# Kernel tuning notes

Measured on AMD Instinct MI355X. Metric: run time of the kernel, lower is better.

## Reference

```python
import jax, jax.numpy as jnp
import numpy as np

B, T, D = 2, 2048, 2048
H, KVH = 16, 4
HD = D // H            # 128 head_dim
D1 = HD // 2           # 64 tied (no-rope) dims
D2 = HD - D1           # 64 rope dims
REP = H // KVH         # 4 kv repeats
ROPE_BASE = 10000.0
EPS = 1e-6
LAMBDA_INIT = 0.8 - 0.6 * float(np.exp(-0.3 * 0))  # layer_depth=0 -> 0.2


def setup_inputs() -> dict:
    key = jax.random.key(0)
    ks = jax.random.split(key, 8)
    x = jax.random.normal(ks[0], (B, T, D), jnp.float32)
    W_qkv = jax.random.normal(ks[1], (D, (H + KVH) * HD), jnp.float32) * 0.02
    W_rope_k = jax.random.normal(ks[2], (D, D2), jnp.float32) * 0.02
    b_rope_k = jnp.zeros((D2,), jnp.float32)
    softmax_scaler = jnp.ones((H,), jnp.float32)
    lambda_q1 = jax.random.normal(ks[3], (D1,), jnp.float32) * 0.1
    lambda_k1 = jax.random.normal(ks[4], (D1,), jnp.float32) * 0.1
    lambda_q2 = jax.random.normal(ks[5], (D1,), jnp.float32) * 0.1
    lambda_k2 = jax.random.normal(ks[6], (D1,), jnp.float32) * 0.1
    return {"hidden_states": x, "W_qkv": W_qkv, "W_rope_k": W_rope_k,
            "b_rope_k": b_rope_k, "softmax_scaler": softmax_scaler,
            "lambda_q1": lambda_q1, "lambda_k1": lambda_k1,
            "lambda_q2": lambda_q2, "lambda_k2": lambda_k2}


def _rmsnorm(x):
    return x * jax.lax.rsqrt(jnp.mean(x * x, axis=-1, keepdims=True) + EPS)


def _rope_tables(seq_len):
    inv_freq = 1.0 / ROPE_BASE ** (jnp.arange(0, D2, 2, dtype=jnp.float32) / D2)
    t = jnp.arange(seq_len, dtype=jnp.float32)
    freqs = jnp.outer(t, inv_freq)          # [T, D2/2]
    return jnp.cos(freqs), jnp.sin(freqs)


def _apply_rotary(x, cos, sin):
    # x: [B, T, h, D2]; cos/sin: [T, D2/2]
    d = x.shape[-1] // 2
    x1, x2 = x[..., :d], x[..., d:]
    c = cos[None, :, None, :]
    s = sin[None, :, None, :]
    return jnp.concatenate([x1 * c + x2 * s, -x1 * s + x2 * c], axis=-1)


def _causal_attn(q, k, v):
    # q,k: [B, T, h, HD]; v: [B, T, h, 2*HD]
    scale = 1.0 / jnp.sqrt(jnp.float32(HD))
    scores = jnp.einsum('bthd,bshd->bhts', q, k) * scale
    mask = jnp.arange(T)[:, None] >= jnp.arange(T)[None, :]
    scores = jnp.where(mask[None, None], scores, jnp.float32(-1e30))
    p = jax.nn.softmax(scores, axis=-1)
    return jnp.einsum('bhts,bshd->bthd', p, v)


def reference(hidden_states, W_qkv, W_rope_k, b_rope_k, softmax_scaler,
              lambda_q1, lambda_k1, lambda_q2, lambda_k2):
    x = hidden_states
    qkv = (x @ W_qkv).reshape(B, T, H + KVH, HD)
    qkv = _rmsnorm(qkv)                              # qk_norm (no affine)
    q, kv = qkv[:, :, :H], qkv[:, :, H:]             # [B,T,H,HD], [B,T,KVH,HD]

    q_tied, q_rope = q[..., :D1], q[..., D1:]
    k_rope = (x @ W_rope_k + b_rope_k)[:, :, None, :]          # [B,T,1,D2]
    k_rope = jnp.broadcast_to(k_rope, (B, T, H, D2))

    cos, sin = _rope_tables(T)
    q_rope = _apply_rotary(q_rope, cos, sin)
    k_rope = _apply_rotary(k_rope, cos, sin)
    q = jnp.concatenate([q_tied, q_rope], axis=-1)             # [B,T,H,HD]

    kv_tied, v_hidden = kv[..., :D1], kv[..., D1:]
    kv_tied = jnp.repeat(kv_tied, REP, axis=2)                 # grouped KV
    v_hidden = jnp.repeat(v_hidden, REP, axis=2)
    k = jnp.concatenate([kv_tied, k_rope], axis=-1)            # [B,T,H,HD]
    v = jnp.concatenate([kv_tied, v_hidden], axis=-1)          # [B,T,H,HD]

    # scalable softmax: q <- s_h * log(pos) * q  (full context, wsize=-1)
    pos = jnp.arange(1, T + 1, dtype=jnp.float32)
    q = softmax_scaler[None, None, :, None] * jnp.log(pos)[None, :, None, None] * q

    # differential head pairing
    q1, q2 = q[:, :, 0::2], q[:, :, 1::2]
    k1, k2 = k[:, :, 0::2], k[:, :, 1::2]
    v_pair = v.reshape(B, T, H // 2, 2 * HD)

    y1 = _causal_attn(q1, k1, v_pair)
    y2 = _causal_attn(q2, k2, v_pair)

    lam1 = jnp.exp(jnp.sum(lambda_q1 * lambda_k1))
    lam2 = jnp.exp(jnp.sum(lambda_q2 * lambda_k2))
    lambda_full = lam1 - lam2 + jnp.float32(LAMBDA_INIT)
    y = y1 - lambda_full * y2                                  # [B,T,H/2,2*HD]
    return y
```

## Files before the change

kernel.cpp:

```cpp
#include <hip/hip_runtime.h>

#define TT 2048
#define NQKV 2560

typedef _Float16 f16;
typedef _Float16 f16x8 __attribute__((ext_vector_type(8)));
typedef _Float16 f16x4v __attribute__((ext_vector_type(4)));
typedef _Float16 f16x2 __attribute__((ext_vector_type(2)));
typedef float f32x4 __attribute__((ext_vector_type(4)));

#define GLOBAL_AS(p) ((const __attribute__((address_space(1))) void*)(p))
#define LDS_AS(p)    ((__attribute__((address_space(3))) void*)(p))

__device__ __forceinline__ f32x4 mfma_f16(f16x8 a, f16x8 b, f32x4 c) {
  return __builtin_amdgcn_mfma_f32_16x16x32_f16(a, b, c, 0, 0, 0);
}

__global__ __launch_bounds__(256) void k_cast_f16(const float* __restrict__ in,
                                                  f16* __restrict__ out, int n4) {
  int i = blockIdx.x * 256 + threadIdx.x;
  if (i >= n4) return;
  float4 v = reinterpret_cast<const float4*>(in)[i];
  f16x4v o;
  o[0] = (f16)v.x; o[1] = (f16)v.y; o[2] = (f16)v.z; o[3] = (f16)v.w;
  reinterpret_cast<f16x4v*>(out)[i] = o;
}

__global__ __launch_bounds__(256) void k_transpose_f16(const float* __restrict__ W,
                                                       f16* __restrict__ Wt,
                                                       int K, int N) {
  __shared__ f16 tile[32][33];
  int tx = threadIdx.x & 31, ty = threadIdx.x >> 5;
  int n0 = blockIdx.x * 32, k0 = blockIdx.y * 32;
  #pragma unroll
  for (int i = ty; i < 32; i += 8)
    tile[i][tx] = (f16)W[(size_t)(k0 + i) * N + n0 + tx];
  __syncthreads();
  #pragma unroll
  for (int i = ty; i < 32; i += 8)
    Wt[(size_t)(n0 + i) * K + k0 + tx] = tile[tx][i];
}

template<int BM, int BN, int WGM, int WGN>
__global__ __launch_bounds__(256) void gemm_bt_kernel(
    const f16* __restrict__ A, const f16* __restrict__ Bt,
    f16* __restrict__ C, int M, int N, int K)
{
  constexpr int BK = 32;
  constexpr int WM = BM / WGM, WN = BN / WGN;
  constexpr int FM = WM / 16, FN = WN / 16;
  constexpr int ACH = BM * 4;
  constexpr int TCH = (BM + BN) * 4;
  __shared__ alignas(16) f16 lds[(BM + BN) * BK];
  const int tid = threadIdx.x;
  const int lane = tid & 63;
  const int w = tid >> 6;
  const int l15 = lane & 15, grp = lane >> 4;
  const int wm = w / WGN, wn = w % WGN;
  const int m0 = blockIdx.y * BM, n0 = blockIdx.x * BN;

  f32x4 acc[FM][FN];
  #pragma unroll
  for (int i = 0; i < FM; ++i)
    #pragma unroll
    for (int j = 0; j < FN; ++j)
      acc[i][j] = (f32x4){0.f, 0.f, 0.f, 0.f};

  const int nk = K / BK;
  for (int kt = 0; kt < nk; ++kt) {
    __syncthreads();
    for (int c = tid; c < TCH; c += 256) {
      const f16* gp;
      if (c < ACH) {
        int row = c >> 2;
        gp = A + (size_t)(m0 + row) * K + kt * BK + (c & 3) * 8;
      } else {
        int cc = c - ACH;
        int row = cc >> 2;
        gp = Bt + (size_t)(n0 + row) * K + kt * BK + (cc & 3) * 8;
      }
      __builtin_amdgcn_global_load_lds(GLOBAL_AS(gp),
                                       LDS_AS((char*)lds + (size_t)c * 16),
                                       16, 0, 0);
    }
    __syncthreads();
    f16x8 af[FM], bfr[FN];
    #pragma unroll
    for (int i = 0; i < FM; ++i)
      af[i] = *reinterpret_cast<const f16x8*>(
          (const char*)lds + (size_t)(wm * WM + i * 16 + l15) * 64 + grp * 16);
    #pragma unroll
    for (int j = 0; j < FN; ++j)
      bfr[j] = *reinterpret_cast<const f16x8*>(
          (const char*)lds + (size_t)(BM + wn * WN + j * 16 + l15) * 64 + grp * 16);
    #pragma unroll
    for (int i = 0; i < FM; ++i)
      #pragma unroll
      for (int j = 0; j < FN; ++j)
        acc[i][j] = mfma_f16(af[i], bfr[j], acc[i][j]);
  }
  #pragma unroll
  for (int i = 0; i < FM; ++i)
    #pragma unroll
    for (int j = 0; j < FN; ++j)
      #pragma unroll
      for (int r = 0; r < 4; ++r) {
        int row = m0 + wm * WM + i * 16 + grp * 4 + r;
        int col = n0 + wn * WN + j * 16 + l15;
        C[(size_t)row * N + col] = (f16)acc[i][j][r];
      }
}

__global__ void k_lambda(const float* __restrict__ lq1, const float* __restrict__ lk1,
                         const float* __restrict__ lq2, const float* __restrict__ lk2,
                         float* __restrict__ lam) {
  int lane = threadIdx.x;
  float a = lq1[lane] * lk1[lane];
  float c = lq2[lane] * lk2[lane];
  #pragma unroll
  for (int m = 1; m < 64; m <<= 1) {
    a += __shfl_xor(a, m);
    c += __shfl_xor(c, m);
  }
  if (lane == 0) lam[0] = expf(a) - expf(c) + 0.2f;
}

__global__ __launch_bounds__(256) void k_build(
    const f16* __restrict__ qkv, const f16* __restrict__ krope,
    const float* __restrict__ brope, const float* __restrict__ scaler,
    f16* __restrict__ Qo, f16* __restrict__ Ko, f16* __restrict__ Vto)
{
  const int blk = blockIdx.x;
  const int b = blk >> 11, t = blk & 2047;
  const int tid = threadIdx.x;
  const int lane = tid & 63, w = tid >> 6;
  __shared__ float nrm[20][128];
  __shared__ float cs[32], sn[32];
  if (tid < 32) {
    const float inv = expf(-(float)(2 * tid) * (9.210340371976184f / 64.0f));
    const float fr = (float)t * inv;
    cs[tid] = cosf(fr);
    sn[tid] = sinf(fr);
  }
  const f16* row = qkv + (size_t)blk * NQKV;
  #pragma unroll
  for (int i = 0; i < 5; ++i) {
    const int hh = w + 4 * i;
    f16x2 v = *reinterpret_cast<const f16x2*>(row + hh * 128 + lane * 2);
    float vx = (float)v[0], vy = (float)v[1];
    float ss = vx * vx + vy * vy;
    #pragma unroll
    for (int m = 1; m < 64; m <<= 1) ss += __shfl_xor(ss, m);
    const float r = rsqrtf(ss * (1.0f / 128.0f) + 1e-6f);
    nrm[hh][lane * 2]     = vx * r;
    nrm[hh][lane * 2 + 1] = vy * r;
  }
  __syncthreads();
  const float lg = logf((float)(t + 1));
  {
    const int h = tid >> 4, dc = (tid & 15) * 8;
    const float sc = scaler[h] * lg * 0.08838834764831845f;
    f16x8 ov;
    if (dc < 64) {
      #pragma unroll
      for (int j = 0; j < 8; ++j) ov[j] = (f16)(nrm[h][dc + j] * sc);
    } else if (dc < 96) {
      #pragma unroll
      for (int j = 0; j < 8; ++j) {
        int jj = dc - 64 + j;
        ov[j] = (f16)((nrm[h][64 + jj] * cs[jj] + nrm[h][96 + jj] * sn[jj]) * sc);
      }
    } else {
      #pragma unroll
      for (int j = 0; j < 8; ++j) {
        int jj = dc - 96 + j;
        ov[j] = (f16)((-nrm[h][64 + jj] * sn[jj] + nrm[h][96 + jj] * cs[jj]) * sc);
      }
    }
    *reinterpret_cast<f16x8*>(Qo + ((size_t)(b * 16 + h) * TT + t) * 128 + dc) = ov;
  }
  if (tid < 64) {
    const int gg = tid >> 4, dc = (tid & 15) * 8;
    f16x8 ov;
    if (dc < 64) {
      #pragma unroll
      for (int j = 0; j < 8; ++j) ov[j] = (f16)nrm[16 + gg][dc + j];
    } else if (dc < 96) {
      #pragma unroll
      for (int j = 0; j < 8; ++j) {
        int jj = dc - 64 + j;
        float k1v = (float)krope[(size_t)blk * 64 + jj] + brope[jj];
        float k2v = (float)krope[(size_t)blk * 64 + 32 + jj] + brope[32 + jj];
        ov[j] = (f16)(k1v * cs[jj] + k2v * sn[jj]);
      }
    } else {
      #pragma unroll
      for (int j = 0; j < 8; ++j) {
        int jj = dc - 96 + j;
        float k1v = (float)krope[(size_t)blk * 64 + jj] + brope[jj];
        float k2v = (float)krope[(size_t)blk * 64 + 32 + jj] + brope[32 + jj];
        ov[j] = (f16)(-k1v * sn[jj] + k2v * cs[jj]);
      }
    }
    *reinterpret_cast<f16x8*>(Ko + ((size_t)(b * 4 + gg) * TT + t) * 128 + dc) = ov;
  }
  for (int i = tid; i < 512; i += 256) {
    const int gg = i >> 7, d = i & 127;
    Vto[((size_t)(b * 4 + gg) * 128 + d) * TT + t] = (f16)nrm[16 + gg][d];
  }
}

__global__ __launch_bounds__(128) void flash_kernel(
    const f16* __restrict__ Q, const f16* __restrict__ Kt,
    const f16* __restrict__ Vt, const float* __restrict__ lamp,
    float* __restrict__ out)
{
  const int tid = threadIdx.x;
  const int w = tid >> 6;
  const int lane = tid & 63;
  const int l15 = lane & 15, grp = lane >> 4;
  const int qt = blockIdx.x;
  const int p  = blockIdx.y;
  const int b  = blockIdx.z;
  const int g  = p >> 1;
  const int qbase = qt * 16;

  __shared__ alignas(16) f16 Plds[2][2][16][40];
  __shared__ float Mbuf[2][4][64];
  __shared__ float Lbuf[2][4][64];
  __shared__ f16   Obuf[2][8][4][64];

  f16x8 qf[2][4];
  #pragma unroll
  for (int hh = 0; hh < 2; ++hh) {
    const f16* qp = Q + ((size_t)(b * 16 + 2 * p + hh) * TT + qbase + l15) * 128 + grp * 8;
    #pragma unroll
    for (int kc = 0; kc < 4; ++kc) qf[hh][kc] = *reinterpret_cast<const f16x8*>(qp + kc * 32);
  }

  f32x4 o[2][8];
  #pragma unroll
  for (int hh = 0; hh < 2; ++hh)
    #pragma unroll
    for (int cb = 0; cb < 8; ++cb) o[hh][cb] = (f32x4){0.f, 0.f, 0.f, 0.f};
  float mrow[2][4], lrow[2][4];
  #pragma unroll
  for (int hh = 0; hh < 2; ++hh)
    #pragma unroll
    for (int r = 0; r < 4; ++r) { mrow[hh][r] = -1e30f; lrow[hh][r] = 0.f; }

  const f16* kb = Kt + (size_t)(b * 4 + g) * TT * 128;
  const f16* vb = Vt + (size_t)(b * 4 + g) * 128 * TT;

  const int ntt = qt / 2 + 1;
  const int h   = (ntt + 1) >> 1;
  const int it0 = (w == 0) ? 0 : h;
  const int it1 = (w == 0) ? h : ntt;
  for (int it = it0; it < it1; ++it) {
    const int s0 = it * 32;
    f32x4 s[2][2];
    #pragma unroll
    for (int hh = 0; hh < 2; ++hh)
      #pragma unroll
      for (int st = 0; st < 2; ++st) s[hh][st] = (f32x4){0.f, 0.f, 0.f, 0.f};
    #pragma unroll
    for (int st = 0; st < 2; ++st) {
      #pragma unroll
      for (int kc = 0; kc < 4; ++kc) {
        f16x8 kf = *reinterpret_cast<const f16x8*>(
            kb + (size_t)(s0 + st * 16 + l15) * 128 + kc * 32 + grp * 8);
        s[0][st] = mfma_f16(qf[0][kc], kf, s[0][st]);
        s[1][st] = mfma_f16(qf[1][kc], kf, s[1][st]);
      }
    }
    if (s0 + 31 > qbase) {
      #pragma unroll
      for (int st = 0; st < 2; ++st) {
        const int sidx = s0 + st * 16 + l15;
        #pragma unroll
        for (int r = 0; r < 4; ++r) {
          if (sidx > qbase + grp * 4 + r) { s[0][st][r] = -1e30f; s[1][st][r] = -1e30f; }
        }
      }
    }
    #pragma unroll
    for (int hh = 0; hh < 2; ++hh) {
      float fsc[4];
      int need = 0;
      #pragma unroll
      for (int r = 0; r < 4; ++r) {
        float mx = fmaxf(s[hh][0][r], s[hh][1][r]);
        mx = fmaxf(mx, __shfl_xor(mx, 1));
        mx = fmaxf(mx, __shfl_xor(mx, 2));
        mx = fmaxf(mx, __shfl_xor(mx, 4));
        mx = fmaxf(mx, __shfl_xor(mx, 8));
        const float mnew = fmaxf(mrow[hh][r], mx);
        fsc[r] = __expf(mrow[hh][r] - mnew);
        mrow[hh][r] = mnew;
        const float p0 = __expf(s[hh][0][r] - mnew);
        const float p1 = __expf(s[hh][1][r] - mnew);
        float rs = p0 + p1;
        rs += __shfl_xor(rs, 1);
        rs += __shfl_xor(rs, 2);
        rs += __shfl_xor(rs, 4);
        rs += __shfl_xor(rs, 8);
        lrow[hh][r] = lrow[hh][r] * fsc[r] + rs;
        Plds[w][hh][grp * 4 + r][l15]      = (f16)p0;
        Plds[w][hh][grp * 4 + r][16 + l15] = (f16)p1;
        need |= (fsc[r] != 1.f);
      }
      if (__any(need)) {
        #pragma unroll
        for (int cb = 0; cb < 8; ++cb)
          #pragma unroll
          for (int r = 0; r < 4; ++r) o[hh][cb][r] *= fsc[r];
      }
    }
    asm volatile("s_waitcnt lgkmcnt(0)" ::: "memory");
    f16x8 pa0 = *reinterpret_cast<const f16x8*>(&Plds[w][0][l15][grp * 8]);
    f16x8 pa1 = *reinterpret_cast<const f16x8*>(&Plds[w][1][l15][grp * 8]);
    #pragma unroll
    for (int cb = 0; cb < 8; ++cb) {
      f16x8 vf = *reinterpret_cast<const f16x8*>(
          vb + (size_t)(cb * 16 + l15) * TT + s0 + grp * 8);
      o[0][cb] = mfma_f16(pa0, vf, o[0][cb]);
      o[1][cb] = mfma_f16(pa1, vf, o[1][cb]);
    }
  }
  if (w == 1) {
    #pragma unroll
    for (int hh = 0; hh < 2; ++hh)
      #pragma unroll
      for (int r = 0; r < 4; ++r) {
        Mbuf[hh][r][lane] = mrow[hh][r];
        Lbuf[hh][r][lane] = lrow[hh][r];
        const float inv = lrow[hh][r] > 0.f ? 1.f / lrow[hh][r] : 0.f;
        #pragma unroll
        for (int cb = 0; cb < 8; ++cb)
          Obuf[hh][cb][r][lane] = (f16)(o[hh][cb][r] * inv);
      }
  }
  __syncthreads();
  if (w == 0) {
    const float lam = lamp[0];
    float A0[2][4], W1[2][4], invd[2][4];
    #pragma unroll
    for (int hh = 0; hh < 2; ++hh)
      #pragma unroll
      for (int r = 0; r < 4; ++r) {
        const float m1 = Mbuf[hh][r][lane];
        const float l1 = Lbuf[hh][r][lane];
        const float M = fmaxf(mrow[hh][r], m1);
        const float a0 = __expf(mrow[hh][r] - M);
        const float w1 = __expf(m1 - M) * l1;
        A0[hh][r] = a0;
        W1[hh][r] = w1;
        invd[hh][r] = 1.f / (a0 * lrow[hh][r] + w1);
      }
    #pragma unroll
    for (int cb = 0; cb < 8; ++cb) {
      #pragma unroll
      for (int r = 0; r < 4; ++r) {
        const float y0 = (A0[0][r] * o[0][cb][r] +
                          W1[0][r] * (float)Obuf[0][cb][r][lane]) * invd[0][r];
        const float y1 = (A0[1][r] * o[1][cb][r] +
                          W1[1][r] * (float)Obuf[1][cb][r][lane]) * invd[1][r];
        const float y = y0 - lam * y1;
        const int t = qbase + grp * 4 + r;
        const size_t base = (((size_t)b * TT + t) * 8 + p) * 256 + cb * 16 + l15;
        out[base] = y;
        out[base + 128] = y;
      }
    }
  }
}

extern "C" void kernel_launch(void* const* d_in, const int* in_sizes, int n_in,
                              void* d_out, int out_size, void* d_ws, size_t ws_size,
                              hipStream_t stream) {
  (void)out_size; (void)ws_size;
  int ix = 0, iwq = 1, iwr = 2, isc = 4;
  int idx64[8]; int n64 = 0;
  for (int i = 0; i < n_in; ++i) {
    if (in_sizes[i] == 8388608) ix = i;
    else if (in_sizes[i] == 5242880) iwq = i;
    else if (in_sizes[i] == 131072) iwr = i;
    else if (in_sizes[i] == 16) isc = i;
    else if (in_sizes[i] == 64 && n64 < 8) idx64[n64++] = i;
  }
  int ibr = 3, ilq1 = 5, ilk1 = 6, ilq2 = 7, ilk2 = 8;
  if (n64 == 5) { ibr = idx64[0]; ilq1 = idx64[1]; ilk1 = idx64[2]; ilq2 = idx64[3]; ilk2 = idx64[4]; }

  const float* x   = (const float*)d_in[ix];
  const float* Wq  = (const float*)d_in[iwq];
  const float* Wr  = (const float*)d_in[iwr];
  const float* br  = (const float*)d_in[ibr];
  const float* sc  = (const float*)d_in[isc];
  const float* lq1 = (const float*)d_in[ilq1];
  const float* lk1 = (const float*)d_in[ilk1];
  const float* lq2 = (const float*)d_in[ilq2];
  const float* lk2 = (const float*)d_in[ilk2];
  float* out = (float*)d_out;

  char* ws = (char*)d_ws;
  f16*   xb    = (f16*)  (ws + 0);
  f16*   wtq   = (f16*)  (ws + 16777216);
  f16*   wtr   = (f16*)  (ws + 27262976);
  f16*   qkv16 = (f16*)  (ws + 27525120);
  f16*   kro16 = (f16*)  (ws + 48496640);
  float* lam   = (float*)(ws + 49020928);
  f16*   Qo    = (f16*)  (ws + 0);
  f16*   Ko    = (f16*)  (ws + 16777216);
  f16*   Vto   = (f16*)  (ws + 20971520);

  k_cast_f16<<<dim3(8192), dim3(256), 0, stream>>>(x, xb, 2097152);
  k_transpose_f16<<<dim3(80, 64), dim3(256), 0, stream>>>(Wq, wtq, 2048, 2560);
  k_transpose_f16<<<dim3(2, 64), dim3(256), 0, stream>>>(Wr, wtr, 2048, 64);
  gemm_bt_kernel<128, 128, 2, 2><<<dim3(20, 32), dim3(256), 0, stream>>>(
      xb, wtq, qkv16, 4096, 2560, 2048);
  gemm_bt_kernel<128, 64, 4, 1><<<dim3(1, 32), dim3(256), 0, stream>>>(
      xb, wtr, kro16, 4096, 64, 2048);
  k_lambda<<<dim3(1), dim3(64), 0, stream>>>(lq1, lk1, lq2, lk2, lam);
  k_build<<<dim3(4096), dim3(256), 0, stream>>>(qkv16, kro16, br, sc, Qo, Ko, Vto);
  flash_kernel<<<dim3(128, 8, 2), dim3(128), 0, stream>>>(Qo, Ko, Vto, lam, out);
}
```

Measured before the change: 362.4 us.

## Split flash attention KV loop across four waves with interleaved tiles

The flash kernel now runs four waves per block instead of two. Each wave processes every fourth KV tile rather than a contiguous half. Waves 1-3 write their partial max, sum and normalized output to shared memory, and wave 0 merges all four partials before the differential combine. The goal is to shorten the per-block serial KV loop and raise wave-level parallelism, at the cost of more LDS and a larger merge epilogue.

```diff
diff --git a/kernel.cpp b/kernel.cpp
--- a/kernel.cpp
+++ b/kernel.cpp
@@ -210,7 +210,7 @@
   }
 }
 
-__global__ __launch_bounds__(128) void flash_kernel(
+__global__ __launch_bounds__(256) void flash_kernel(
     const f16* __restrict__ Q, const f16* __restrict__ Kt,
     const f16* __restrict__ Vt, const float* __restrict__ lamp,
     float* __restrict__ out)
@@ -225,10 +225,10 @@
   const int g  = p >> 1;
   const int qbase = qt * 16;
 
-  __shared__ alignas(16) f16 Plds[2][2][16][40];
-  __shared__ float Mbuf[2][4][64];
-  __shared__ float Lbuf[2][4][64];
-  __shared__ f16   Obuf[2][8][4][64];
+  __shared__ alignas(16) f16 Plds[4][2][16][40];
+  __shared__ float Mbuf[3][2][4][64];
+  __shared__ float Lbuf[3][2][4][64];
+  __shared__ f16   Obuf[3][2][8][4][64];
 
   f16x8 qf[2][4];
   #pragma unroll
@@ -253,10 +253,7 @@
   const f16* vb = Vt + (size_t)(b * 4 + g) * 128 * TT;
 
   const int ntt = qt / 2 + 1;
-  const int h   = (ntt + 1) >> 1;
-  const int it0 = (w == 0) ? 0 : h;
-  const int it1 = (w == 0) ? h : ntt;
-  for (int it = it0; it < it1; ++it) {
+  for (int it = w; it < ntt; it += 4) {
     const int s0 = it * 32;
     f32x4 s[2][2];
     #pragma unroll
@@ -327,45 +324,53 @@
       o[1][cb] = mfma_f16(pa1, vf, o[1][cb]);
     }
   }
-  if (w == 1) {
+  if (w > 0) {
     #pragma unroll
     for (int hh = 0; hh < 2; ++hh)
       #pragma unroll
       for (int r = 0; r < 4; ++r) {
-        Mbuf[hh][r][lane] = mrow[hh][r];
-        Lbuf[hh][r][lane] = lrow[hh][r];
+        Mbuf[w - 1][hh][r][lane] = mrow[hh][r];
+        Lbuf[w - 1][hh][r][lane] = lrow[hh][r];
         const float inv = lrow[hh][r] > 0.f ? 1.f / lrow[hh][r] : 0.f;
         #pragma unroll
         for (int cb = 0; cb < 8; ++cb)
-          Obuf[hh][cb][r][lane] = (f16)(o[hh][cb][r] * inv);
+          Obuf[w - 1][hh][cb][r][lane] = (f16)(o[hh][cb][r] * inv);
       }
   }
   __syncthreads();
   if (w == 0) {
     const float lam = lamp[0];
-    float A0[2][4], W1[2][4], invd[2][4];
-    #pragma unroll
-    for (int hh = 0; hh < 2; ++hh)
+    #pragma unroll
+    for (int hh = 0; hh < 2; ++hh) {
       #pragma unroll
       for (int r = 0; r < 4; ++r) {
-        const float m1 = Mbuf[hh][r][lane];
-        const float l1 = Lbuf[hh][r][lane];
-        const float M = fmaxf(mrow[hh][r], m1);
+        float M = mrow[hh][r];
+        #pragma unroll
+        for (int j = 0; j < 3; ++j) M = fmaxf(M, Mbuf[j][hh][r][lane]);
         const float a0 = __expf(mrow[hh][r] - M);
-        const float w1 = __expf(m1 - M) * l1;
-        A0[hh][r] = a0;
-        W1[hh][r] = w1;
-        invd[hh][r] = 1.f / (a0 * lrow[hh][r] + w1);
-      }
+        float wj[3];
+        float den = a0 * lrow[hh][r];
+        #pragma unroll
+        for (int j = 0; j < 3; ++j) {
+          wj[j] = __expf(Mbuf[j][hh][r][lane] - M) * Lbuf[j][hh][r][lane];
+          den += wj[j];
+        }
+        const float inv = 1.f / den;
+        #pragma unroll
+        for (int cb = 0; cb < 8; ++cb) {
+          float y = a0 * o[hh][cb][r];
+          #pragma unroll
+          for (int j = 0; j < 3; ++j)
+            y += wj[j] * (float)Obuf[j][hh][cb][r][lane];
+          o[hh][cb][r] = y * inv;
+        }
+      }
+    }
     #pragma unroll
     for (int cb = 0; cb < 8; ++cb) {
       #pragma unroll
       for (int r = 0; r < 4; ++r) {
-        const float y0 = (A0[0][r] * o[0][cb][r] +
-                          W1[0][r] * (float)Obuf[0][cb][r][lane]) * invd[0][r];
-        const float y1 = (A0[1][r] * o[1][cb][r] +
-                          W1[1][r] * (float)Obuf[1][cb][r][lane]) * invd[1][r];
-        const float y = y0 - lam * y1;
+        const float y = o[0][cb][r] - lam * o[1][cb][r];
         const int t = qbase + grp * 4 + r;
         const size_t base = (((size_t)b * TT + t) * 8 + p) * 256 + cb * 16 + l15;
         out[base] = y;
@@ -422,5 +427,5 @@
       xb, wtr, kro16, 4096, 64, 2048);
   k_lambda<<<dim3(1), dim3(64), 0, stream>>>(lq1, lk1, lq2, lk2, lam);
   k_build<<<dim3(4096), dim3(256), 0, stream>>>(qkv16, kro16, br, sc, Qo, Ko, Vto);
-  flash_kernel<<<dim3(128, 8, 2), dim3(128), 0, stream>>>(Qo, Ko, Vto, lam, out);
-}
+  flash_kernel<<<dim3(128, 8, 2), dim3(256), 0, stream>>>(Qo, Ko, Vto, lam, out);
+}
```

Result: slower. 441.7 us (+21.9%).
